# Performance work log

Measured on AMD Instinct MI355X. Metric: run time of the kernel, lower is better.

## Reference

```python
import jax, jax.numpy as jnp
import numpy as np

B, S, D = 2, 1024, 2048
H, DN, DR, DV, R = 16, 128, 64, 128, 512
E, K, FI, SI = 12, 4, 1408, 2816
THETA = 10000.0
EPS = 1e-6


def rmsnorm(x, w):
    return x * jax.lax.rsqrt(jnp.mean(x * x, -1, keepdims=True) + EPS) * w


def rope(x, cos, sin):
    # interleaved-pair rotation (torch view_as_complex convention)
    x1, x2 = x[..., 0::2], x[..., 1::2]
    return jnp.stack([x1 * cos - x2 * sin, x1 * sin + x2 * cos], axis=-1).reshape(x.shape)


def setup_inputs() -> dict:
    key = jax.random.key(0)
    ks = jax.random.split(key, 16)
    w = lambda k, sh: jax.random.normal(k, sh, jnp.float32) * 0.02
    inp = {
        'x': jax.random.normal(ks[0], (B, S, D), jnp.float32),
        'wq': w(ks[1], (D, H * (DN + DR))),
        'wkv_a': w(ks[2], (D, R + DR)),
        'kv_norm_w': jnp.ones((R,), jnp.float32),
        'wkv_b': w(ks[3], (R, H * (DN + DV))),
        'wo': w(ks[4], (H * DV, D)),
        'norm_w': jnp.ones((D,), jnp.float32),
        'gate_w': w(ks[5], (D, E)),
        'gate_b': jnp.zeros((E,), jnp.float32),
        'w1': w(ks[6], (E, D, FI)),
        'w2': w(ks[7], (E, FI, D)),
        'w3': w(ks[8], (E, D, FI)),
        'ws1': w(ks[9], (D, SI)),
        'ws2': w(ks[10], (SI, D)),
        'ws3': w(ks[11], (D, SI)),
        'mask': jnp.triu(jnp.full((S, S), -1e9, jnp.float32), 1),  # causal
        'start_pos': 0,
    }
    return inp


def reference(x, wq, wkv_a, kv_norm_w, wkv_b, wo, norm_w, gate_w, gate_b,
              w1, w2, w3, ws1, ws2, ws3, mask, start_pos):
    def mla(h):
        q = (h @ wq).reshape(B, S, H, DN + DR)
        q_nope, q_pe = q[..., :DN], q[..., DN:]
        kv = h @ wkv_a                              # [B,S,R+DR]
        kv_lat = rmsnorm(kv[..., :R], kv_norm_w)    # latent KV (kv_lora_rank)
        k_pe = kv[..., R:]                          # [B,S,DR] shared across heads
        kvb = (kv_lat @ wkv_b).reshape(B, S, H, DN + DV)
        k_nope, v = kvb[..., :DN], kvb[..., DN:]
        pos = start_pos + jnp.arange(S)
        inv = 1.0 / (THETA ** (jnp.arange(0, DR, 2, dtype=jnp.float32) / DR))
        ang = pos[:, None].astype(jnp.float32) * inv[None, :]
        cos, sin = jnp.cos(ang), jnp.sin(ang)       # [S, DR//2]
        q_pe = rope(q_pe, cos[None, :, None, :], sin[None, :, None, :])
        k_pe = rope(k_pe, cos[None, :, :], sin[None, :, :])
        scale = (DN + DR) ** -0.5
        scores = (jnp.einsum('bshd,bthd->bhst', q_nope, k_nope)
                  + jnp.einsum('bshd,btd->bhst', q_pe, k_pe)) * scale
        scores = scores + mask[None, None, :, :]
        p = jax.nn.softmax(scores, axis=-1)
        o = jnp.einsum('bhst,bthd->bshd', p, v).reshape(B, S, H * DV)
        return o @ wo

    def moe(h):
        t = h.reshape(-1, D)                        # [T, D]
        T = t.shape[0]
        s = jax.nn.sigmoid(t @ gate_w)              # routing scores [T, E]
        _, topi = jax.lax.top_k(s + gate_b[None, :], K)   # adaptive bias only for selection
        wgt = jnp.take_along_axis(s, topi, axis=1)
        wgt = wgt / jnp.sum(wgt, -1, keepdims=True)
        route = jnp.zeros((T, E), t.dtype).at[jnp.arange(T)[:, None], topi].set(wgt)
        hh = jnp.einsum('td,edi->eti', t, w1)
        gg = jax.nn.silu(hh) * jnp.einsum('td,edi->eti', t, w3)
        eo = jnp.einsum('eti,eid->etd', gg, w2)
        out = jnp.einsum('te,etd->td', route, eo)
        shared = (jax.nn.silu(t @ ws1) * (t @ ws3)) @ ws2
        return (out + shared).reshape(B, S, D)

    first = mla(rmsnorm(x, norm_w)) + x
    return moe(rmsnorm(first, norm_w)) + first
```

## Files before the change

### kernel.cpp

```cpp
#include <hip/hip_runtime.h>
#include <math.h>

typedef unsigned short u16;
typedef __attribute__((ext_vector_type(8))) short short8;
typedef __attribute__((ext_vector_type(8))) _Float16 half8;
typedef __attribute__((ext_vector_type(4))) float f32x4;

__device__ inline u16 f32_to_bf16_rne(float f){
    unsigned int u = __float_as_uint(f);
    unsigned int r = (u + 0x7FFFu + ((u >> 16) & 1u)) >> 16;
    return (u16)r;
}
__device__ inline float bf16_to_f32(u16 h){ return __uint_as_float(((unsigned int)h) << 16); }
__device__ inline u16 h2b(_Float16 h){ union { _Float16 f; u16 u; } x; x.f = h; return x.u; }

__device__ __forceinline__ void glds16(const void* g, void* l){
    __builtin_amdgcn_global_load_lds((const __attribute__((address_space(1))) void*)g,
                                     (__attribute__((address_space(3))) void*)l, 16, 0, 0);
}
#define WAIT_VM0()  { asm volatile("s_waitcnt vmcnt(0)" ::: "memory"); __builtin_amdgcn_sched_barrier(0); }
#define WAIT_LGKM0() { asm volatile("s_waitcnt lgkmcnt(0)" ::: "memory"); __builtin_amdgcn_sched_barrier(0); }
#define RAW_BAR()   { __builtin_amdgcn_s_barrier(); __builtin_amdgcn_sched_barrier(0); }

#define TT 2048
#define DD 2048
#define SS 1024
#define NH 16

#define EPI_F32     0
#define EPI_BF16    1
#define EPI_RES     2
#define EPI_SILUMUL 3
#define EPI_F16PAIR 4
#define EPI_QROPE   5

template<int PAIR>
__global__ __launch_bounds__(256) void cvtT_k(const float* __restrict__ W, long long wstr,
        u16* __restrict__ WTh, u16* __restrict__ WTl, long long tstr, int K, int Nsrc){
    __shared__ float L[64][65];
    int e = blockIdx.z;
    const float* Wp = W + (long long)e * wstr;
    int k0 = blockIdx.y * 64, n0 = blockIdx.x * 64;
    int tid = threadIdx.x;
#pragma unroll
    for (int it = 0; it < 4; ++it) {
        int r = (tid >> 4) + it * 16, cc = (tid & 15) * 4;
        int col = n0 + cc;
        float4 v = {0.f, 0.f, 0.f, 0.f};
        if (col + 3 < Nsrc) v = *(const float4*)(Wp + (long long)(k0 + r) * Nsrc + col);
        else {
            const float* p = Wp + (long long)(k0 + r) * Nsrc;
            float tmp[4] = {0.f, 0.f, 0.f, 0.f};
#pragma unroll
            for (int q2 = 0; q2 < 4; q2++) if (col + q2 < Nsrc) tmp[q2] = p[col + q2];
            v.x = tmp[0]; v.y = tmp[1]; v.z = tmp[2]; v.w = tmp[3];
        }
        L[r][cc] = v.x; L[r][cc+1] = v.y; L[r][cc+2] = v.z; L[r][cc+3] = v.w;
    }
    __syncthreads();
#pragma unroll
    for (int it = 0; it < 2; ++it) {
        int idx = it * 256 + tid; int n = idx >> 3, kc = (idx & 7) * 8;
        u16 hi[8], lo[8];
#pragma unroll
        for (int u = 0; u < 8; ++u) {
            float v = L[kc + u][n];
            if (PAIR) { _Float16 h = (_Float16)v; hi[u] = h2b(h); lo[u] = h2b((_Float16)(v - (float)h)); }
            else hi[u] = f32_to_bf16_rne(v);
        }
        long long o = (long long)e * tstr + (long long)(n0 + n) * K + k0 + kc;
        *(short8*)(WTh + o) = *(short8*)hi;
        if (PAIR) *(short8*)(WTl + o) = *(short8*)lo;
    }
}

template<int EPI, bool PREC, bool AGLDS>
__global__ __launch_bounds__(256) void gemm_k(
    const u16* __restrict__ A0, const u16* __restrict__ A1, int lda,
    const u16* __restrict__ BTh, const u16* __restrict__ BTl, long long btstr,
    int M, int N, int K,
    const int* offs, const int* cnt, const int* gather, int ebase,
    void* C0, void* C1, int ldc,
    const void* aux, const float* __restrict__ cosT, const float* __restrict__ sinT,
    int zsplit)
{
    __shared__ u16 AsH[2][4096];
    __shared__ u16 AsL[PREC ? 2 : 1][PREC ? 4096 : 8];
    __shared__ u16 BsH[2][4096];
    __shared__ u16 BsL[PREC ? 2 : 1][PREC ? 4096 : 8];

    int tid  = threadIdx.x;
    int lane = tid & 63;
    int wv   = tid >> 6;
    int wm = (wv >> 1) * 64, wn = (wv & 1) * 64;

    int Lid = blockIdx.y * gridDim.x + blockIdx.x;
    int jj  = Lid >> 3;
    int yb  = jj % gridDim.y;
    int nb  = (Lid & 7) + ((jj / gridDim.y) << 3);
    int n0 = nb * 128;
    if (n0 >= N) return;

    int zz   = blockIdx.z;
    int e    = ebase + ((zsplit > 0 && zz >= zsplit) ? (zz - zsplit) : zz);
    int base = offs ? offs[e] : 0;
    int mc   = cnt ? cnt[e] : M;
    int m0   = yb * 128;
    if (m0 >= mc) return;
    const u16* Bh = BTh + (long long)zz * btstr;
    const u16* Bl = PREC ? (BTl + (long long)zz * btstr) : (const u16*)nullptr;
    void* Cw = (zsplit > 0 && zz >= zsplit) ? C1 : C0;

    int rr_ = tid >> 2, s4 = tid & 3;
    long long arow0 = -1, arow1 = -1;
    if (!AGLDS) {
        if (m0 + rr_ < mc)      arow0 = gather ? (long long)gather[base + m0 + rr_]      : (long long)(base + m0 + rr_);
        if (m0 + rr_ + 64 < mc) arow1 = gather ? (long long)gather[base + m0 + rr_ + 64] : (long long)(base + m0 + rr_ + 64);
    }

    f32x4 acc[4][4];
#pragma unroll
    for (int i = 0; i < 4; i++)
#pragma unroll
        for (int j = 0; j < 4; j++) { f32x4 z = {0.f,0.f,0.f,0.f}; acc[i][j] = z; }

    short8 zer = {0,0,0,0,0,0,0,0};
    short8 a0h = zer, a1h = zer, a0l = zer, a1l = zer;

    int gr0 = wv * 16 + (lane >> 2);
    int gsl = lane & 3;

#define STAGE_GL(PB, KT)                                                         \
    {                                                                            \
        _Pragma("unroll")                                                        \
        for (int it = 0; it < 2; ++it) {                                         \
            int r = it * 64 + gr0;                                               \
            int s = gsl ^ ((r >> 1) & 3);                                        \
            glds16(Bh + (long long)(n0 + r) * K + (KT) + s * 8,                  \
                   (char*)&BsH[PB][0] + it * 4096 + wv * 1024);                  \
            if (PREC)                                                            \
                glds16(Bl + (long long)(n0 + r) * K + (KT) + s * 8,              \
                       (char*)&BsL[PB][0] + it * 4096 + wv * 1024);              \
            if (AGLDS) {                                                         \
                glds16(A0 + (long long)(base + m0 + r) * lda + (KT) + s * 8,     \
                       (char*)&AsH[PB][0] + it * 4096 + wv * 1024);              \
                if (PREC)                                                        \
                    glds16(A1 + (long long)(base + m0 + r) * lda + (KT) + s * 8, \
                           (char*)&AsL[PB][0] + it * 4096 + wv * 1024);          \
            }                                                                    \
        }                                                                        \
        if (!AGLDS) {                                                            \
            a0h = (arow0 >= 0) ? *(const short8*)(A0 + arow0 * lda + (KT) + s4 * 8) : zer; \
            a1h = (arow1 >= 0) ? *(const short8*)(A0 + arow1 * lda + (KT) + s4 * 8) : zer; \
            if (PREC) {                                                          \
                a0l = (arow0 >= 0) ? *(const short8*)(A1 + arow0 * lda + (KT) + s4 * 8) : zer; \
                a1l = (arow1 >= 0) ? *(const short8*)(A1 + arow1 * lda + (KT) + s4 * 8) : zer; \
            }                                                                    \
        }                                                                        \
    }

    int pb = 0;
    STAGE_GL(0, 0);
    for (int kt = 0; kt < K; kt += 32) {
        WAIT_VM0();
        if (!AGLDS) {
            int d0 = rr_ * 64 + 16 * (s4 ^ ((rr_ >> 1) & 3));
            int r1w = rr_ + 64;
            int d1 = r1w * 64 + 16 * (s4 ^ ((r1w >> 1) & 3));
            *(short8*)((char*)&AsH[pb][0] + d0) = a0h;
            *(short8*)((char*)&AsH[pb][0] + d1) = a1h;
            if (PREC) {
                *(short8*)((char*)&AsL[pb][0] + d0) = a0l;
                *(short8*)((char*)&AsL[pb][0] + d1) = a1l;
            }
            WAIT_LGKM0();
        }
        RAW_BAR();
        if (kt + 32 < K) { STAGE_GL(pb ^ 1, kt + 32); }
        if (PREC) {
            half8 ah[4], al[4];
#pragma unroll
            for (int i = 0; i < 4; i++) {
                int ra = wm + i * 16 + (lane & 15);
                int off = ra * 64 + 16 * ((lane >> 4) ^ ((ra >> 1) & 3));
                ah[i] = *(const half8*)((const char*)&AsH[pb][0] + off);
                al[i] = *(const half8*)((const char*)&AsL[pb][0] + off);
            }
#pragma unroll
            for (int j = 0; j < 4; j++) {
                int rb = wn + j * 16 + (lane & 15);
                int off = rb * 64 + 16 * ((lane >> 4) ^ ((rb >> 1) & 3));
                half8 bh = *(const half8*)((const char*)&BsH[pb][0] + off);
                half8 bl = *(const half8*)((const char*)&BsL[pb][0] + off);
#pragma unroll
                for (int i = 0; i < 4; i++) {
                    acc[i][j] = __builtin_amdgcn_mfma_f32_16x16x32_f16(ah[i], bh, acc[i][j], 0, 0, 0);
                    acc[i][j] = __builtin_amdgcn_mfma_f32_16x16x32_f16(ah[i], bl, acc[i][j], 0, 0, 0);
                    acc[i][j] = __builtin_amdgcn_mfma_f32_16x16x32_f16(al[i], bh, acc[i][j], 0, 0, 0);
                }
            }
        } else {
            short8 af[4];
#pragma unroll
            for (int i = 0; i < 4; i++) {
                int ra = wm + i * 16 + (lane & 15);
                af[i] = *(const short8*)((const char*)&AsH[pb][0] + ra * 64 + 16 * ((lane >> 4) ^ ((ra >> 1) & 3)));
            }
#pragma unroll
            for (int j = 0; j < 4; j++) {
                int rb = wn + j * 16 + (lane & 15);
                short8 bfr = *(const short8*)((const char*)&BsH[pb][0] + rb * 64 + 16 * ((lane >> 4) ^ ((rb >> 1) & 3)));
#pragma unroll
                for (int i = 0; i < 4; i++)
                    acc[i][j] = __builtin_amdgcn_mfma_f32_16x16x32_bf16(af[i], bfr, acc[i][j], 0, 0, 0);
            }
        }
        pb ^= 1;
    }
#undef STAGE_GL

    if (EPI == EPI_QROPE) {
#pragma unroll
        for (int i = 0; i < 4; i++) {
            int rr0 = m0 + wm + i * 16 + ((lane >> 4) << 2);
#pragma unroll
            for (int j = 0; j < 4; j++) {
                int col = n0 + wn + j * 16 + (lane & 15);
                int hd = col % 192;
#pragma unroll
                for (int r = 0; r < 4; r++) {
                    int rr = rr0 + r;
                    float v = acc[i][j][r];
                    float pv = __shfl_xor(v, 1);
                    float outv = v;
                    if (hd >= 128) {
                        int s = rr & (SS - 1);
                        int pi2 = (hd - 128) >> 1;
                        float cc_ = cosT[s * 32 + pi2], sn_ = sinT[s * 32 + pi2];
                        bool odd = col & 1;
                        float a0 = odd ? pv : v, a1 = odd ? v : pv;
                        outv = odd ? (a0 * sn_ + a1 * cc_) : (a0 * cc_ - a1 * sn_);
                    }
                    long long cidx = (long long)rr * ldc + col;
                    _Float16 hh = (_Float16)outv;
                    ((u16*)C0)[cidx] = h2b(hh);
                    ((u16*)C1)[cidx] = h2b((_Float16)(outv - (float)hh));
                }
            }
        }
    } else {
#pragma unroll
        for (int i = 0; i < 4; i++) {
            int rbase = m0 + wm + i * 16 + ((lane >> 4) << 2);
#pragma unroll
            for (int j = 0; j < 4; j++) {
                int col = n0 + wn + j * 16 + (lane & 15);
                if (col >= N) continue;
#pragma unroll
                for (int r = 0; r < 4; r++) {
                    int rr = rbase + r;
                    if (rr >= mc) continue;
                    long long cidx = (long long)(base + rr) * ldc + col;
                    float v = acc[i][j][r];
                    if (EPI == EPI_F32)      ((float*)C0)[cidx] = v;
                    else if (EPI == EPI_BF16) ((u16*)Cw)[cidx] = f32_to_bf16_rne(v);
                    else if (EPI == EPI_RES)  ((float*)C0)[cidx] = v + ((const float*)aux)[cidx];
                    else if (EPI == EPI_SILUMUL) {
                        float h1v = bf16_to_f32(((const u16*)aux)[cidx]);
                        float g = h1v / (1.f + __expf(-h1v)) * v;
                        ((u16*)C0)[cidx] = f32_to_bf16_rne(g);
                    } else {
                        _Float16 hh = (_Float16)v;
                        ((u16*)C0)[cidx] = h2b(hh);
                        ((u16*)C1)[cidx] = h2b((_Float16)(v - (float)hh));
                    }
                }
            }
        }
    }
}

__global__ __launch_bounds__(256) void silumul_k(u16* __restrict__ g, const u16* __restrict__ h3,
                                                 long long n){
    long long i = ((long long)blockIdx.x * 256 + threadIdx.x) * 8;
    if (i >= n) return;
    short8 a = *(const short8*)(g + i);
    short8 b = *(const short8*)(h3 + i);
    u16 o[8];
#pragma unroll
    for (int u = 0; u < 8; ++u) {
        float x = bf16_to_f32((u16)a[u]);
        float y = bf16_to_f32((u16)b[u]);
        o[u] = f32_to_bf16_rne(x / (1.f + __expf(-x)) * y);
    }
    *(short8*)(g + i) = *(short8*)o;
}

__global__ void costab_k(const int* sp, float* ct, float* st){
    int idx = blockIdx.x * 256 + threadIdx.x;
    if (idx >= SS * 32) return;
    int i = idx & 31, s = idx >> 5;
    float inv = powf(10000.0f, -(float)i / 32.0f);
    float a = (float)(sp[0] + s) * inv;
    ct[idx] = cosf(a);
    st[idx] = sinf(a);
}

template<int MODE>
__global__ __launch_bounds__(256) void rms_k(const float* __restrict__ x, const float* __restrict__ w,
                                             u16* o0, u16* o1){
    int t = blockIdx.x, tid = threadIdx.x;
    const float* row = x + (long long)t * DD;
    float4 v0 = *(const float4*)(row + tid * 4);
    float4 v1 = *(const float4*)(row + 1024 + tid * 4);
    float ss = v0.x*v0.x + v0.y*v0.y + v0.z*v0.z + v0.w*v0.w
             + v1.x*v1.x + v1.y*v1.y + v1.z*v1.z + v1.w*v1.w;
#pragma unroll
    for (int d = 1; d < 64; d <<= 1) ss += __shfl_xor(ss, d, 64);
    __shared__ float red[4];
    if ((tid & 63) == 0) red[tid >> 6] = ss;
    __syncthreads();
    float sc = rsqrtf((red[0] + red[1] + red[2] + red[3]) / (float)DD + 1e-6f);
    float a[8];
    a[0]=v0.x; a[1]=v0.y; a[2]=v0.z; a[3]=v0.w; a[4]=v1.x; a[5]=v1.y; a[6]=v1.z; a[7]=v1.w;
#pragma unroll
    for (int q2 = 0; q2 < 8; q2++) {
        int d = (q2 < 4) ? (tid * 4 + q2) : (1024 + tid * 4 + (q2 - 4));
        float y = a[q2] * sc * w[d];
        if (MODE == 0) {
            _Float16 hh = (_Float16)y;
            o0[(long long)t * DD + d] = h2b(hh);
            o1[(long long)t * DD + d] = h2b((_Float16)(y - (float)hh));
        } else {
            o0[(long long)t * DD + d] = f32_to_bf16_rne(y);
        }
    }
}

__global__ __launch_bounds__(256) void kvprep_k(const float* __restrict__ kv, const float* __restrict__ kw,
    const float* __restrict__ ct, const float* __restrict__ st,
    u16* lath, u16* latl, u16* kpeh, u16* kpel){
    int t = blockIdx.x, tid = threadIdx.x;
    const float* row = kv + (long long)t * 576;
    float x0 = row[tid], x1 = row[256 + tid];
    float ss = x0 * x0 + x1 * x1;
#pragma unroll
    for (int d = 1; d < 64; d <<= 1) ss += __shfl_xor(ss, d, 64);
    __shared__ float red[4];
    if ((tid & 63) == 0) red[tid >> 6] = ss;
    __syncthreads();
    float sc = rsqrtf((red[0] + red[1] + red[2] + red[3]) / 512.f + 1e-6f);
    float y0 = x0 * sc * kw[tid], y1 = x1 * sc * kw[256 + tid];
    _Float16 h0 = (_Float16)y0, h1 = (_Float16)y1;
    lath[(long long)t * 512 + tid] = h2b(h0);
    latl[(long long)t * 512 + tid] = h2b((_Float16)(y0 - (float)h0));
    lath[(long long)t * 512 + 256 + tid] = h2b(h1);
    latl[(long long)t * 512 + 256 + tid] = h2b((_Float16)(y1 - (float)h1));
    if (tid < 32) {
        int s = t & (SS - 1);
        float a0 = row[512 + 2 * tid], a1 = row[513 + 2 * tid];
        float c = ct[s * 32 + tid], sn = st[s * 32 + tid];
        float r0 = a0 * c - a1 * sn, r1 = a0 * sn + a1 * c;
        _Float16 p0 = (_Float16)r0, p1 = (_Float16)r1;
        kpeh[(long long)t * 64 + 2 * tid]     = h2b(p0);
        kpel[(long long)t * 64 + 2 * tid]     = h2b((_Float16)(r0 - (float)p0));
        kpeh[(long long)t * 64 + 2 * tid + 1] = h2b(p1);
        kpel[(long long)t * 64 + 2 * tid + 1] = h2b((_Float16)(r1 - (float)p1));
    }
}

__global__ __launch_bounds__(256) void vtprep_k(const u16* __restrict__ kvbh, const u16* __restrict__ kvbl,
                                                u16* vth, u16* vtl){
    __shared__ u16 L[64][136];
    int bh = blockIdx.x, st = blockIdx.y, pl = blockIdx.z;
    const u16* src = pl ? kvbl : kvbh;
    u16* dst = pl ? vtl : vth;
    int b = bh >> 4, hh = bh & 15;
    int tid = threadIdx.x;
#pragma unroll
    for (int it = 0; it < 4; ++it) {
        int idx = it * 256 + tid; int sl = idx >> 4, dc = idx & 15;
        long long t = (long long)b * SS + st * 64 + sl;
        *(short8*)&L[sl][dc * 8] = *(const short8*)(src + t * 4096 + hh * 256 + 128 + dc * 8);
    }
    __syncthreads();
#pragma unroll
    for (int it = 0; it < 4; ++it) {
        int idx = it * 256 + tid; int d = idx >> 3, sc = idx & 7;
        short8 v;
#pragma unroll
        for (int u = 0; u < 8; u++) v[u] = (short)L[sc * 8 + u][d];
        *(short8*)(dst + ((long long)bh * 128 + d) * SS + st * 64 + sc * 8) = v;
    }
}

__global__ __launch_bounds__(256) void attn_k(
    const u16* __restrict__ qh_, const u16* __restrict__ ql_,
    const u16* __restrict__ kvbh, const u16* __restrict__ kvbl,
    const u16* __restrict__ kpeh, const u16* __restrict__ kpel,
    const u16* __restrict__ vth, const u16* __restrict__ vtl,
    u16* ohi, u16* olo)
{
    __shared__ u16 KsH[32][200], KsL[32][200];
    __shared__ u16 VsH[128][40], VsL[128][40];
    __shared__ u16 PlH[4][16][40], PlL[4][16][40];
    int bx = blockIdx.x, bh = blockIdx.y;
    int qi = (bh & 16) ? bx : (15 - bx);
    int b = bh >> 4, h = bh & 15;
    int tid = threadIdx.x, lane = tid & 63, wv = tid >> 6;
    int q0 = qi * 64;
    const u16* vbh = vth + (long long)bh * 128 * SS;
    const u16* vbl = vtl + (long long)bh * 128 * SS;

    half8 qh[6], ql[6];
    {
        int row = q0 + wv * 16 + (lane & 15);
        const u16* ph = qh_ + (long long)(b * SS + row) * 3072 + h * 192 + (lane >> 4) * 8;
        const u16* pl = ql_ + (long long)(b * SS + row) * 3072 + h * 192 + (lane >> 4) * 8;
#pragma unroll
        for (int ks = 0; ks < 6; ks++) {
            qh[ks] = *(const half8*)(ph + ks * 32);
            ql[ks] = *(const half8*)(pl + ks * 32);
        }
    }
    float mrun[4], lrun[4];
    f32x4 oacc[8];
#pragma unroll
    for (int r = 0; r < 4; r++) { mrun[r] = -1e30f; lrun[r] = 0.f; }
#pragma unroll
    for (int f = 0; f < 8; f++) { f32x4 z = {0.f,0.f,0.f,0.f}; oacc[f] = z; }
    const float scale = 0.07216878364870322f;

    short8 kh0, kh1, kh2, kl0, kl1, kl2, vh0, vh1, vl0, vl1;
    int kr0 = tid / 24 + 0,  kc0 = tid % 24;
    int kr1 = (256 + tid) / 24, kc1 = (256 + tid) % 24;
    int kr2 = (512 + tid) / 24, kc2 = (512 + tid) % 24;
    int vr0 = tid >> 2, vc0 = tid & 3;
    int vr1 = (256 + tid) >> 2, vc1 = vc0;

#define ALOAD(T0)                                                                   \
    {                                                                               \
        long long tg0 = (long long)b * SS + (T0);                                   \
        if (kc0 < 16) { kh0 = *(const short8*)(kvbh + (tg0 + kr0) * 4096 + h * 256 + kc0 * 8); \
                        kl0 = *(const short8*)(kvbl + (tg0 + kr0) * 4096 + h * 256 + kc0 * 8); } \
        else          { kh0 = *(const short8*)(kpeh + (tg0 + kr0) * 64 + (kc0 - 16) * 8);      \
                        kl0 = *(const short8*)(kpel + (tg0 + kr0) * 64 + (kc0 - 16) * 8); }    \
        if (kc1 < 16) { kh1 = *(const short8*)(kvbh + (tg0 + kr1) * 4096 + h * 256 + kc1 * 8); \
                        kl1 = *(const short8*)(kvbl + (tg0 + kr1) * 4096 + h * 256 + kc1 * 8); } \
        else          { kh1 = *(const short8*)(kpeh + (tg0 + kr1) * 64 + (kc1 - 16) * 8);      \
                        kl1 = *(const short8*)(kpel + (tg0 + kr1) * 64 + (kc1 - 16) * 8); }    \
        if (kc2 < 16) { kh2 = *(const short8*)(kvbh + (tg0 + kr2) * 4096 + h * 256 + kc2 * 8); \
                        kl2 = *(const short8*)(kvbl + (tg0 + kr2) * 4096 + h * 256 + kc2 * 8); } \
        else          { kh2 = *(const short8*)(kpeh + (tg0 + kr2) * 64 + (kc2 - 16) * 8);      \
                        kl2 = *(const short8*)(kpel + (tg0 + kr2) * 64 + (kc2 - 16) * 8); }    \
        vh0 = *(const short8*)(vbh + (long long)vr0 * SS + (T0) + vc0 * 8);         \
        vl0 = *(const short8*)(vbl + (long long)vr0 * SS + (T0) + vc0 * 8);         \
        vh1 = *(const short8*)(vbh + (long long)vr1 * SS + (T0) + vc1 * 8);         \
        vl1 = *(const short8*)(vbl + (long long)vr1 * SS + (T0) + vc1 * 8);         \
    }

    int ntile = 2 * qi + 2;
    ALOAD(0);
    for (int ti = 0; ti < ntile; ++ti) {
        int t0 = ti * 32;
        WAIT_VM0();
        RAW_BAR();
        *(short8*)&KsH[kr0][kc0 * 8] = kh0; *(short8*)&KsL[kr0][kc0 * 8] = kl0;
        *(short8*)&KsH[kr1][kc1 * 8] = kh1; *(short8*)&KsL[kr1][kc1 * 8] = kl1;
        *(short8*)&KsH[kr2][kc2 * 8] = kh2; *(short8*)&KsL[kr2][kc2 * 8] = kl2;
        *(short8*)&VsH[vr0][vc0 * 8] = vh0; *(short8*)&VsL[vr0][vc0 * 8] = vl0;
        *(short8*)&VsH[vr1][vc1 * 8] = vh1; *(short8*)&VsL[vr1][vc1 * 8] = vl1;
        WAIT_LGKM0();
        RAW_BAR();
        if (ti + 1 < ntile) ALOAD(t0 + 32);
        f32x4 s[2];
#pragma unroll
        for (int nt = 0; nt < 2; ++nt) {
            f32x4 a = {0.f,0.f,0.f,0.f};
#pragma unroll
            for (int ks = 0; ks < 6; ++ks) {
                half8 kh = *(const half8*)&KsH[nt * 16 + (lane & 15)][ks * 32 + (lane >> 4) * 8];
                half8 kl = *(const half8*)&KsL[nt * 16 + (lane & 15)][ks * 32 + (lane >> 4) * 8];
                a = __builtin_amdgcn_mfma_f32_16x16x32_f16(qh[ks], kh, a, 0, 0, 0);
                a = __builtin_amdgcn_mfma_f32_16x16x32_f16(qh[ks], kl, a, 0, 0, 0);
                a = __builtin_amdgcn_mfma_f32_16x16x32_f16(ql[ks], kh, a, 0, 0, 0);
            }
            s[nt] = a;
        }
#pragma unroll
        for (int nt = 0; nt < 2; ++nt)
#pragma unroll
            for (int r = 0; r < 4; ++r) {
                float v = s[nt][r] * scale;
                if (ti >= 2 * qi) {
                    int t = t0 + nt * 16 + (lane & 15);
                    int sq = q0 + wv * 16 + (lane >> 4) * 4 + r;
                    if (t > sq) v = -1e30f;
                }
                s[nt][r] = v;
            }
        float corr[4];
#pragma unroll
        for (int r = 0; r < 4; ++r) {
            float m = fmaxf(s[0][r], s[1][r]);
#pragma unroll
            for (int d = 1; d < 16; d <<= 1) m = fmaxf(m, __shfl_xor(m, d, 64));
            float mn = fmaxf(mrun[r], m);
            corr[r] = __expf(mrun[r] - mn);
            mrun[r] = mn;
        }
        float rs[4] = {0.f, 0.f, 0.f, 0.f};
#pragma unroll
        for (int nt = 0; nt < 2; ++nt)
#pragma unroll
            for (int r = 0; r < 4; ++r) {
                float p = __expf(s[nt][r] - mrun[r]);
                s[nt][r] = p;
                rs[r] += p;
            }
#pragma unroll
        for (int r = 0; r < 4; ++r) {
            float tsum = rs[r];
#pragma unroll
            for (int d = 1; d < 16; d <<= 1) tsum += __shfl_xor(tsum, d, 64);
            lrun[r] = lrun[r] * corr[r] + tsum;
        }
#pragma unroll
        for (int f = 0; f < 8; f++)
#pragma unroll
            for (int r = 0; r < 4; r++) oacc[f][r] *= corr[r];
#pragma unroll
        for (int nt = 0; nt < 2; ++nt)
#pragma unroll
            for (int r = 0; r < 4; ++r) {
                float p = s[nt][r];
                _Float16 ph = (_Float16)p;
                PlH[wv][(lane >> 4) * 4 + r][nt * 16 + (lane & 15)] = h2b(ph);
                PlL[wv][(lane >> 4) * 4 + r][nt * 16 + (lane & 15)] = h2b((_Float16)(p - (float)ph));
            }
        half8 pfh = *(const half8*)&PlH[wv][lane & 15][(lane >> 4) * 8];
        half8 pfl = *(const half8*)&PlL[wv][lane & 15][(lane >> 4) * 8];
#pragma unroll
        for (int f = 0; f < 8; ++f) {
            half8 vh = *(const half8*)&VsH[f * 16 + (lane & 15)][(lane >> 4) * 8];
            half8 vl = *(const half8*)&VsL[f * 16 + (lane & 15)][(lane >> 4) * 8];
            oacc[f] = __builtin_amdgcn_mfma_f32_16x16x32_f16(pfh, vh, oacc[f], 0, 0, 0);
            oacc[f] = __builtin_amdgcn_mfma_f32_16x16x32_f16(pfh, vl, oacc[f], 0, 0, 0);
            oacc[f] = __builtin_amdgcn_mfma_f32_16x16x32_f16(pfl, vh, oacc[f], 0, 0, 0);
        }
    }
#undef ALOAD
#pragma unroll
    for (int f = 0; f < 8; ++f)
#pragma unroll
        for (int r = 0; r < 4; ++r) {
            int sq = q0 + wv * 16 + (lane >> 4) * 4 + r;
            float v = oacc[f][r] / lrun[r];
            _Float16 hh = (_Float16)v;
            long long o = ((long long)(b * SS + sq)) * 2048 + h * 128 + f * 16 + (lane & 15);
            ohi[o] = h2b(hh);
            olo[o] = h2b((_Float16)(v - (float)hh));
        }
}

__global__ __launch_bounds__(256) void gate_k(const float* __restrict__ first,
    const float* __restrict__ nw, const float* __restrict__ gw, const float* __restrict__ gb,
    int* topi, float* wgt){
    int wv = threadIdx.x >> 6, lane = threadIdx.x & 63;
    int t = blockIdx.x * 4 + wv;
    const float* row = first + (long long)t * DD;
    float rv[32];
    float ss = 0.f;
#pragma unroll
    for (int it = 0; it < 32; ++it) {
        float v = row[it * 64 + lane];
        rv[it] = v;
        ss += v * v;
    }
#pragma unroll
    for (int d = 1; d < 64; d <<= 1) ss += __shfl_xor(ss, d, 64);
    float sc = rsqrtf(ss / (float)DD + 1e-6f);
    float acc[12];
#pragma unroll
    for (int e = 0; e < 12; e++) acc[e] = 0.f;
#pragma unroll
    for (int it = 0; it < 32; ++it) {
        int i = it * 64 + lane;
        float v = rv[it] * sc * nw[i];
        const float* g = gw + (long long)i * 12;
        float4 g0 = *(const float4*)g;
        float4 g1 = *(const float4*)(g + 4);
        float4 g2 = *(const float4*)(g + 8);
        acc[0] += v * g0.x; acc[1] += v * g0.y; acc[2]  += v * g0.z; acc[3]  += v * g0.w;
        acc[4] += v * g1.x; acc[5] += v * g1.y; acc[6]  += v * g1.z; acc[7]  += v * g1.w;
        acc[8] += v * g2.x; acc[9] += v * g2.y; acc[10] += v * g2.z; acc[11] += v * g2.w;
    }
#pragma unroll
    for (int e = 0; e < 12; e++)
#pragma unroll
        for (int d = 1; d < 64; d <<= 1) acc[e] += __shfl_xor(acc[e], d, 64);
    if (lane == 0) {
        float s[12], rank[12];
#pragma unroll
        for (int e = 0; e < 12; e++) { s[e] = 1.f / (1.f + expf(-acc[e])); rank[e] = s[e] + gb[e]; }
        int sel[4]; float wv4[4]; float wsum = 0.f;
#pragma unroll
        for (int k = 0; k < 4; k++) {
            int bi = 0; float bv = -1e30f;
#pragma unroll
            for (int e = 0; e < 12; e++) if (rank[e] > bv) { bv = rank[e]; bi = e; }
            sel[k] = bi; rank[bi] = -1e31f;
            wv4[k] = s[bi]; wsum += s[bi];
        }
#pragma unroll
        for (int k = 0; k < 4; k++) {
            topi[t * 4 + k] = sel[k];
            wgt[t * 4 + k] = wv4[k] / wsum;
        }
    }
}

__global__ __launch_bounds__(256) void offs_k(const int* __restrict__ topi,
                                              int* cnt, int* offs, int* cur){
    __shared__ int lh[4][12];
    int tid = threadIdx.x, wv = tid >> 6, lane = tid & 63;
    int c[12];
#pragma unroll
    for (int e = 0; e < 12; e++) c[e] = 0;
    for (int i = tid; i < TT * 4; i += 256) {
        int e = topi[i];
#pragma unroll
        for (int q = 0; q < 12; q++) c[q] += (e == q) ? 1 : 0;
    }
#pragma unroll
    for (int e = 0; e < 12; e++) {
        int v = c[e];
#pragma unroll
        for (int d = 1; d < 64; d <<= 1) v += __shfl_xor(v, d, 64);
        if (lane == 0) lh[wv][e] = v;
    }
    __syncthreads();
    if (tid == 0) {
        int a = 0;
        for (int e = 0; e < 12; e++) {
            int tot = lh[0][e] + lh[1][e] + lh[2][e] + lh[3][e];
            cnt[e] = tot; offs[e] = a; a += tot; cur[e] = 0;
        }
        offs[12] = a;
    }
}

__global__ __launch_bounds__(256) void scatter_k(const int* __restrict__ topi,
    const float* __restrict__ wgt, const int* __restrict__ offs,
    int* cur, int* tok, float* wgl, int* posm){
    __shared__ int lh[12];
    __shared__ int gb[12];
    int tid = threadIdx.x;
    if (tid < 12) lh[tid] = 0;
    __syncthreads();
    int t = blockIdx.x * 256 + tid;
    int e4[4], lr[4];
#pragma unroll
    for (int k = 0; k < 4; k++) {
        e4[k] = topi[t * 4 + k];
        lr[k] = atomicAdd(&lh[e4[k]], 1);
    }
    __syncthreads();
    if (tid < 12) gb[tid] = atomicAdd(&cur[tid], lh[tid]);
    __syncthreads();
#pragma unroll
    for (int k = 0; k < 4; k++) {
        int pos = offs[e4[k]] + gb[e4[k]] + lr[k];
        tok[pos] = t;
        wgl[pos] = wgt[t * 4 + k];
        posm[t * 4 + k] = pos;
    }
}

__global__ void final_k(const float* __restrict__ first, const u16* __restrict__ so,
    const u16* __restrict__ eo, const int* __restrict__ posm, const float* __restrict__ wgl,
    float* out){
    int idx = blockIdx.x * 256 + threadIdx.x;
    int d4 = idx & 511, t = idx >> 9;
    int d = d4 * 4;
    const float* fp = first + (long long)t * DD + d;
    const u16* sp = so + (long long)t * DD + d;
    float r0 = fp[0] + bf16_to_f32(sp[0]);
    float r1 = fp[1] + bf16_to_f32(sp[1]);
    float r2 = fp[2] + bf16_to_f32(sp[2]);
    float r3 = fp[3] + bf16_to_f32(sp[3]);
#pragma unroll
    for (int k = 0; k < 4; k++) {
        int pos = posm[t * 4 + k];
        float wv = wgl[pos];
        const u16* ep = eo + (long long)pos * DD + d;
        r0 += wv * bf16_to_f32(ep[0]);
        r1 += wv * bf16_to_f32(ep[1]);
        r2 += wv * bf16_to_f32(ep[2]);
        r3 += wv * bf16_to_f32(ep[3]);
    }
    float4 res = {r0, r1, r2, r3};
    *(float4*)(out + (long long)t * DD + d) = res;
}

extern "C" void kernel_launch(void* const* d_in, const int* in_sizes, int n_in,
                              void* d_out, int out_size, void* d_ws, size_t ws_size,
                              hipStream_t stream)
{
    const float* x       = (const float*)d_in[0];
    const float* wq      = (const float*)d_in[1];
    const float* wkv_a   = (const float*)d_in[2];
    const float* kvnw    = (const float*)d_in[3];
    const float* wkv_b   = (const float*)d_in[4];
    const float* wo      = (const float*)d_in[5];
    const float* norm_w  = (const float*)d_in[6];
    const float* gate_w  = (const float*)d_in[7];
    const float* gate_b  = (const float*)d_in[8];
    const float* w1      = (const float*)d_in[9];
    const float* w2      = (const float*)d_in[10];
    const float* w3      = (const float*)d_in[11];
    const float* ws1     = (const float*)d_in[12];
    const float* ws2     = (const float*)d_in[13];
    const float* ws3     = (const float*)d_in[14];
    const int*   startp  = (const int*)d_in[16];
    char* ws = (char*)d_ws;

    const size_t O_COS = 0, O_SIN = 131072, O_KPEH = 262144, O_KPEL = 524288;
    const size_t O_TOPI = 786432, O_WGT = 819200, O_TOK = 851968, O_WGL = 884736, O_POSM = 917504;
    const size_t O_CNT = 950272, O_OFFS = 950336, O_CUR = 950400;
    const size_t O_WB = 1048576;
    const size_t B2 = 26214400;
    const size_t O_H    = B2,             O_HLO  = B2 + 8388608;
    const size_t O_Q    = B2 + 16777216,  O_QLO  = B2 + 29360128;
    const size_t O_KVF  = B2 + 41943040;
    const size_t O_LATH = B2 + 46661632,  O_LATL = B2 + 48758784;
    const size_t O_KVBH = B2 + 50855936,  O_KVBL = B2 + 67633152;
    const size_t O_VTH  = B2,             O_VTL  = B2 + 8388608;
    const size_t O_OH   = B2 + 84410368,  O_OL   = B2 + 92798976;
    const size_t O_FIRST= B2 + 16777216;
    const size_t O_TBF  = B2;
    const size_t O_H1   = B2 + 33554432;
    const size_t O_EO   = B2 + 56623104;
    const size_t O_SH1  = B2 + 90177536;
    const size_t O_SO   = B2 + 101711872;

    float* cosT = (float*)(ws + O_COS);  float* sinT = (float*)(ws + O_SIN);
    u16* kpeh = (u16*)(ws + O_KPEH);     u16* kpel = (u16*)(ws + O_KPEL);
    int* topi = (int*)(ws + O_TOPI);     float* wgt = (float*)(ws + O_WGT);
    int* tok = (int*)(ws + O_TOK);       float* wgl = (float*)(ws + O_WGL);
    int* posm = (int*)(ws + O_POSM);
    int* cntp = (int*)(ws + O_CNT); int* offsp = (int*)(ws + O_OFFS); int* curp = (int*)(ws + O_CUR);
    u16* WB   = (u16*)(ws + O_WB);
    u16* hhi = (u16*)(ws + O_H);    u16* hlo = (u16*)(ws + O_HLO);
    u16* qhp = (u16*)(ws + O_Q);    u16* qlp = (u16*)(ws + O_QLO);
    float* kvf = (float*)(ws + O_KVF);
    u16* lath = (u16*)(ws + O_LATH); u16* latl = (u16*)(ws + O_LATL);
    u16* kvbh = (u16*)(ws + O_KVBH); u16* kvbl = (u16*)(ws + O_KVBL);
    u16* vth = (u16*)(ws + O_VTH);  u16* vtl = (u16*)(ws + O_VTL);
    u16* oh  = (u16*)(ws + O_OH);   u16* ol  = (u16*)(ws + O_OL);
    float* first = (float*)(ws + O_FIRST);
    u16* tbf = (u16*)(ws + O_TBF);
    u16* h1buf = (u16*)(ws + O_H1); u16* eo = (u16*)(ws + O_EO);
    u16* sh1 = (u16*)(ws + O_SH1);  u16* sobuf = (u16*)(ws + O_SO);
    u16* sh3 = (u16*)(ws + O_H1);

    costab_k<<<128, 256, 0, stream>>>(startp, cosT, sinT);
    rms_k<0><<<TT, 256, 0, stream>>>(x, norm_w, hhi, hlo);

    cvtT_k<1><<<dim3(48, 32, 1), 256, 0, stream>>>(wq, 0, WB, WB + 6291456, 0, 2048, 3072);
    gemm_k<EPI_QROPE, true, true><<<dim3(24, 16, 1), 256, 0, stream>>>(
        hhi, hlo, 2048, WB, WB + 6291456, 0, 2048, 3072, 2048,
        nullptr, nullptr, nullptr, 0, qhp, qlp, 3072, nullptr, cosT, sinT, 0);

    cvtT_k<1><<<dim3(10, 32, 1), 256, 0, stream>>>(wkv_a, 0, WB, WB + 1310720, 0, 2048, 576);
    gemm_k<EPI_F32, true, true><<<dim3(8, 16, 1), 256, 0, stream>>>(
        hhi, hlo, 2048, WB, WB + 1310720, 0, 2048, 576, 2048,
        nullptr, nullptr, nullptr, 0, kvf, nullptr, 576, nullptr, nullptr, nullptr, 0);
    kvprep_k<<<TT, 256, 0, stream>>>(kvf, kvnw, cosT, sinT, lath, latl, kpeh, kpel);

    cvtT_k<1><<<dim3(64, 8, 1), 256, 0, stream>>>(wkv_b, 0, WB, WB + 2097152, 0, 512, 4096);
    gemm_k<EPI_F16PAIR, true, true><<<dim3(32, 16, 1), 256, 0, stream>>>(
        lath, latl, 512, WB, WB + 2097152, 0, 2048, 4096, 512,
        nullptr, nullptr, nullptr, 0, kvbh, kvbl, 4096, nullptr, nullptr, nullptr, 0);

    vtprep_k<<<dim3(32, 16, 2), 256, 0, stream>>>(kvbh, kvbl, vth, vtl);
    attn_k<<<dim3(16, 32, 1), 256, 0, stream>>>(qhp, qlp, kvbh, kvbl, kpeh, kpel, vth, vtl, oh, ol);

    cvtT_k<1><<<dim3(32, 32, 1), 256, 0, stream>>>(wo, 0, WB, WB + 4194304, 0, 2048, 2048);
    gemm_k<EPI_RES, true, true><<<dim3(16, 16, 1), 256, 0, stream>>>(
        oh, ol, 2048, WB, WB + 4194304, 0, 2048, 2048, 2048,
        nullptr, nullptr, nullptr, 0, first, nullptr, 2048, x, nullptr, nullptr, 0);

    rms_k<1><<<TT, 256, 0, stream>>>(first, norm_w, tbf, nullptr);
    gate_k<<<512, 256, 0, stream>>>(first, norm_w, gate_w, gate_b, topi, wgt);
    offs_k<<<1, 256, 0, stream>>>(topi, cntp, offsp, curp);
    scatter_k<<<8, 256, 0, stream>>>(topi, wgt, offsp, curp, tok, wgl, posm);

    const long long SW = (long long)2816 * 2048;
    cvtT_k<0><<<dim3(44, 32, 1), 256, 0, stream>>>(ws1, 0, WB, nullptr, 0, 2048, 2816);
    cvtT_k<0><<<dim3(44, 32, 1), 256, 0, stream>>>(ws3, 0, WB + SW, nullptr, 0, 2048, 2816);
    gemm_k<EPI_BF16, false, true><<<dim3(24, 16, 2), 256, 0, stream>>>(
        tbf, nullptr, 2048, WB, nullptr, SW, 2048, 2816, 2048,
        nullptr, nullptr, nullptr, 0, sh1, sh3, 2816, nullptr, nullptr, nullptr, 1);
    silumul_k<<<2816, 256, 0, stream>>>(sh1, sh3, (long long)2048 * 2816);
    cvtT_k<0><<<dim3(32, 44, 1), 256, 0, stream>>>(ws2, 0, WB, nullptr, 0, 2816, 2048);
    gemm_k<EPI_BF16, false, true><<<dim3(16, 16, 1), 256, 0, stream>>>(
        sh1, nullptr, 2816, WB, nullptr, 0, 2048, 2048, 2816,
        nullptr, nullptr, nullptr, 0, sobuf, nullptr, 2048, nullptr, nullptr, nullptr, 0);

    const long long EW = (long long)2048 * 1408;
    for (int g = 0; g < 3; ++g) {
        cvtT_k<0><<<dim3(22, 32, 4), 256, 0, stream>>>(w1 + (long long)g * 4 * EW, EW, WB, nullptr, EW, 2048, 1408);
        gemm_k<EPI_BF16, false, false><<<dim3(16, 16, 4), 256, 0, stream>>>(
            tbf, nullptr, 2048, WB, nullptr, EW, 2048, 1408, 2048,
            offsp, cntp, tok, 4 * g, h1buf, nullptr, 1408, nullptr, nullptr, nullptr, 0);
        cvtT_k<0><<<dim3(22, 32, 4), 256, 0, stream>>>(w3 + (long long)g * 4 * EW, EW, WB, nullptr, EW, 2048, 1408);
        gemm_k<EPI_SILUMUL, false, false><<<dim3(16, 16, 4), 256, 0, stream>>>(
            tbf, nullptr, 2048, WB, nullptr, EW, 2048, 1408, 2048,
            offsp, cntp, tok, 4 * g, h1buf, nullptr, 1408, h1buf, nullptr, nullptr, 0);
        cvtT_k<0><<<dim3(32, 22, 4), 256, 0, stream>>>(w2 + (long long)g * 4 * EW, EW, WB, nullptr, EW, 1408, 2048);
        gemm_k<EPI_BF16, false, true><<<dim3(16, 16, 4), 256, 0, stream>>>(
            h1buf, nullptr, 1408, WB, nullptr, EW, 2048, 2048, 1408,
            offsp, cntp, nullptr, 4 * g, eo, nullptr, 2048, nullptr, nullptr, nullptr, 0);
    }

    final_k<<<4096, 256, 0, stream>>>(first, sobuf, eo, posm, wgl, (float*)d_out);
}
```

Before: 1.328 ms.

## Add specialized bf16 GEMM with direct-register A loads for MoE and shared FFN

Adds a new GEMM kernel for the single-precision-split-free bf16 paths. It stages only the B tile into LDS via global_load_lds with a swizzled layout, and loads A fragments straight from global memory into registers, with optional row gather for routed experts. It double-buffers in 32-wide K steps. It replaces the generic gemm_k in the shared expert and routed expert GEMMs, aiming to cut LDS traffic and barriers. The risk is uncoalesced, gathered A loads from global memory and lower A reuse across waves.

```diff
diff --git a/kernel.cpp b/kernel.cpp
--- a/kernel.cpp
+++ b/kernel.cpp
@@ -280,6 +280,135 @@
     }
 }
 
+template<int EPI, bool GATHER>
+__global__ __launch_bounds__(256) void gemmb_k(
+    const u16* __restrict__ A0, int lda,
+    const u16* __restrict__ BTh, long long btstr,
+    int M, int N, int K,
+    const int* offs, const int* cnt, const int* gather, int ebase,
+    void* C0, void* C1, int ldc,
+    const void* aux, int zsplit)
+{
+    __shared__ u16 Bs[2][4096];
+
+    int tid  = threadIdx.x;
+    int lane = tid & 63;
+    int wv   = tid >> 6;
+    int wm = (wv >> 1) * 64, wn = (wv & 1) * 64;
+
+    int Lid = blockIdx.y * gridDim.x + blockIdx.x;
+    int jj  = Lid >> 3;
+    int yb  = jj % gridDim.y;
+    int nb  = (Lid & 7) + ((jj / gridDim.y) << 3);
+    int n0 = nb * 128;
+    if (n0 >= N) return;
+
+    int zz   = blockIdx.z;
+    int e    = ebase + ((zsplit > 0 && zz >= zsplit) ? (zz - zsplit) : zz);
+    int base = offs ? offs[e] : 0;
+    int mc   = cnt ? cnt[e] : M;
+    int m0   = yb * 128;
+    if (m0 >= mc) return;
+    const u16* Bh = BTh + (long long)zz * btstr;
+    void* Cw = (zsplit > 0 && zz >= zsplit) ? C1 : C0;
+
+    long long aoff[4];
+    bool aok[4];
+#pragma unroll
+    for (int i = 0; i < 4; i++) {
+        int row = m0 + wm + i * 16 + (lane & 15);
+        bool ok = row < mc;
+        int rsel = ok ? row : 0;
+        long long rowg;
+        if (GATHER) rowg = (long long)gather[base + rsel];
+        else        rowg = (long long)(base + rsel);
+        aoff[i] = rowg * (long long)lda + ((lane >> 4) * 8);
+        aok[i] = ok;
+    }
+
+    f32x4 acc[4][4];
+#pragma unroll
+    for (int i = 0; i < 4; i++)
+#pragma unroll
+        for (int j = 0; j < 4; j++) { f32x4 z = {0.f,0.f,0.f,0.f}; acc[i][j] = z; }
+
+    short8 zer = {0,0,0,0,0,0,0,0};
+    int gr0 = wv * 16 + (lane >> 2);
+    int gsl = lane & 3;
+
+#define STAGE_B2(PB, KT)                                                         \
+    {                                                                            \
+        _Pragma("unroll")                                                        \
+        for (int it = 0; it < 2; ++it) {                                         \
+            int r = it * 64 + gr0;                                               \
+            int s = gsl ^ ((r >> 1) & 3);                                        \
+            glds16(Bh + (long long)(n0 + r) * K + (KT) + s * 8,                  \
+                   (char*)&Bs[PB][0] + it * 4096 + wv * 1024);                   \
+        }                                                                        \
+    }
+#define ALOADA(DST, KT)                                                          \
+    {                                                                            \
+        _Pragma("unroll")                                                        \
+        for (int i = 0; i < 4; i++) {                                            \
+            short8 v_ = *(const short8*)(A0 + aoff[i] + (KT));                   \
+            DST[i] = aok[i] ? v_ : zer;                                          \
+        }                                                                        \
+    }
+#define COMPUTE_B(AF, PB)                                                        \
+    {                                                                            \
+        _Pragma("unroll")                                                        \
+        for (int j = 0; j < 4; j++) {                                            \
+            int rb = wn + j * 16 + (lane & 15);                                  \
+            short8 bfr = *(const short8*)((const char*)&Bs[PB][0] + rb * 64 + 16 * ((lane >> 4) ^ ((rb >> 1) & 3))); \
+            _Pragma("unroll")                                                    \
+            for (int i = 0; i < 4; i++)                                          \
+                acc[i][j] = __builtin_amdgcn_mfma_f32_16x16x32_bf16(AF[i], bfr, acc[i][j], 0, 0, 0); \
+        }                                                                        \
+    }
+
+    short8 afA[4], afB[4];
+    STAGE_B2(0, 0);
+    ALOADA(afA, 0);
+    for (int kt = 0; kt < K; kt += 64) {
+        WAIT_VM0();
+        RAW_BAR();
+        if (kt + 32 < K) { STAGE_B2(1, kt + 32); ALOADA(afB, kt + 32); }
+        __builtin_amdgcn_sched_barrier(0);
+        COMPUTE_B(afA, 0);
+        WAIT_VM0();
+        RAW_BAR();
+        if (kt + 64 < K) { STAGE_B2(0, kt + 64); ALOADA(afA, kt + 64); }
+        __builtin_amdgcn_sched_barrier(0);
+        COMPUTE_B(afB, 1);
+    }
+#undef STAGE_B2
+#undef ALOADA
+#undef COMPUTE_B
+
+#pragma unroll
+    for (int i = 0; i < 4; i++) {
+        int rbase = m0 + wm + i * 16 + ((lane >> 4) << 2);
+#pragma unroll
+        for (int j = 0; j < 4; j++) {
+            int col = n0 + wn + j * 16 + (lane & 15);
+            if (col >= N) continue;
+#pragma unroll
+            for (int r = 0; r < 4; r++) {
+                int rr = rbase + r;
+                if (rr >= mc) continue;
+                long long cidx = (long long)(base + rr) * ldc + col;
+                float v = acc[i][j][r];
+                if (EPI == EPI_BF16) ((u16*)Cw)[cidx] = f32_to_bf16_rne(v);
+                else {
+                    float h1v = bf16_to_f32(((const u16*)aux)[cidx]);
+                    float g = h1v / (1.f + __expf(-h1v)) * v;
+                    ((u16*)C0)[cidx] = f32_to_bf16_rne(g);
+                }
+            }
+        }
+    }
+}
+
 __global__ __launch_bounds__(256) void silumul_k(u16* __restrict__ g, const u16* __restrict__ h3,
                                                  long long n){
     long long i = ((long long)blockIdx.x * 256 + threadIdx.x) * 8;
@@ -799,29 +928,29 @@
     const long long SW = (long long)2816 * 2048;
     cvtT_k<0><<<dim3(44, 32, 1), 256, 0, stream>>>(ws1, 0, WB, nullptr, 0, 2048, 2816);
     cvtT_k<0><<<dim3(44, 32, 1), 256, 0, stream>>>(ws3, 0, WB + SW, nullptr, 0, 2048, 2816);
-    gemm_k<EPI_BF16, false, true><<<dim3(24, 16, 2), 256, 0, stream>>>(
-        tbf, nullptr, 2048, WB, nullptr, SW, 2048, 2816, 2048,
-        nullptr, nullptr, nullptr, 0, sh1, sh3, 2816, nullptr, nullptr, nullptr, 1);
+    gemmb_k<EPI_BF16, false><<<dim3(24, 16, 2), 256, 0, stream>>>(
+        tbf, 2048, WB, SW, 2048, 2816, 2048,
+        nullptr, nullptr, nullptr, 0, sh1, sh3, 2816, nullptr, 1);
     silumul_k<<<2816, 256, 0, stream>>>(sh1, sh3, (long long)2048 * 2816);
     cvtT_k<0><<<dim3(32, 44, 1), 256, 0, stream>>>(ws2, 0, WB, nullptr, 0, 2816, 2048);
-    gemm_k<EPI_BF16, false, true><<<dim3(16, 16, 1), 256, 0, stream>>>(
-        sh1, nullptr, 2816, WB, nullptr, 0, 2048, 2048, 2816,
-        nullptr, nullptr, nullptr, 0, sobuf, nullptr, 2048, nullptr, nullptr, nullptr, 0);
+    gemmb_k<EPI_BF16, false><<<dim3(16, 16, 1), 256, 0, stream>>>(
+        sh1, 2816, WB, 0, 2048, 2048, 2816,
+        nullptr, nullptr, nullptr, 0, sobuf, nullptr, 2048, nullptr, 0);
 
     const long long EW = (long long)2048 * 1408;
     for (int g = 0; g < 3; ++g) {
         cvtT_k<0><<<dim3(22, 32, 4), 256, 0, stream>>>(w1 + (long long)g * 4 * EW, EW, WB, nullptr, EW, 2048, 1408);
-        gemm_k<EPI_BF16, false, false><<<dim3(16, 16, 4), 256, 0, stream>>>(
-            tbf, nullptr, 2048, WB, nullptr, EW, 2048, 1408, 2048,
-            offsp, cntp, tok, 4 * g, h1buf, nullptr, 1408, nullptr, nullptr, nullptr, 0);
+        gemmb_k<EPI_BF16, true><<<dim3(16, 16, 4), 256, 0, stream>>>(
+            tbf, 2048, WB, EW, 2048, 1408, 2048,
+            offsp, cntp, tok, 4 * g, h1buf, nullptr, 1408, nullptr, 0);
         cvtT_k<0><<<dim3(22, 32, 4), 256, 0, stream>>>(w3 + (long long)g * 4 * EW, EW, WB, nullptr, EW, 2048, 1408);
-        gemm_k<EPI_SILUMUL, false, false><<<dim3(16, 16, 4), 256, 0, stream>>>(
-            tbf, nullptr, 2048, WB, nullptr, EW, 2048, 1408, 2048,
-            offsp, cntp, tok, 4 * g, h1buf, nullptr, 1408, h1buf, nullptr, nullptr, 0);
+        gemmb_k<EPI_SILUMUL, true><<<dim3(16, 16, 4), 256, 0, stream>>>(
+            tbf, 2048, WB, EW, 2048, 1408, 2048,
+            offsp, cntp, tok, 4 * g, h1buf, nullptr, 1408, h1buf, 0);
         cvtT_k<0><<<dim3(32, 22, 4), 256, 0, stream>>>(w2 + (long long)g * 4 * EW, EW, WB, nullptr, EW, 1408, 2048);
-        gemm_k<EPI_BF16, false, true><<<dim3(16, 16, 4), 256, 0, stream>>>(
-            h1buf, nullptr, 1408, WB, nullptr, EW, 2048, 2048, 1408,
-            offsp, cntp, nullptr, 4 * g, eo, nullptr, 2048, nullptr, nullptr, nullptr, 0);
+        gemmb_k<EPI_BF16, false><<<dim3(16, 16, 4), 256, 0, stream>>>(
+            h1buf, 1408, WB, EW, 2048, 2048, 1408,
+            offsp, cntp, nullptr, 4 * g, eo, nullptr, 2048, nullptr, 0);
     }
 
     final_k<<<4096, 256, 0, stream>>>(first, sobuf, eo, posm, wgl, (float*)d_out);
```

Result: slower. 1.693 ms (+27.5%).
